# Kernel optimization log

Measured on AMD Instinct MI355X. Metric: run time of the kernel, lower is better.

## Reference

```python
import jax, jax.numpy as jnp
import numpy as np

B, D, M, C = 8192, 2048, 8, 1000

def setup_inputs() -> dict:
    key = jax.random.key(0)
    k1, k2, k3, k4, k5 = jax.random.split(key, 5)
    scale = 1.0 / np.sqrt(D)
    return {
        "x": jax.random.normal(k1, (B, D), dtype=jnp.float32),
        "model_weights": jax.random.normal(k2, (M, D, C), dtype=jnp.float32) * scale,
        "model_bias": jax.random.normal(k3, (M, C), dtype=jnp.float32) * 0.01,
        "resnet_weight": jax.random.normal(k4, (D, M * C), dtype=jnp.float32) * scale,
        "resnet_bias": jax.random.normal(k5, (M * C,), dtype=jnp.float32) * 0.01,
    }

def reference(x, model_weights, model_bias, resnet_weight, resnet_bias):
    # Per-submodel logits: [B, M, C]
    outputs = jnp.einsum("bd,mdc->bmc", x, model_weights) + model_bias[None, :, :]
    # Fusion weights from the weighting network: [B, M, C]
    w = (x @ resnet_weight + resnet_bias).reshape(x.shape[0], model_weights.shape[0], model_weights.shape[2])
    # Fused weighted sum over models (replaces the triple Python loop): [B, C]
    result = jnp.sum(outputs * w, axis=1)
    return result
```

## Files before the change

kernel.cpp:

```cpp
#include <hip/hip_runtime.h>
#include <hip/hip_bf16.h>
#include <stdint.h>

#define BDIM 8192
#define DDIM 2048
#define MDIM 8
#define CDIM 1000
#define CPAD 1024
#define NPAD 8192

typedef __attribute__((ext_vector_type(8))) short bf16x8;
typedef __attribute__((ext_vector_type(4))) float f32x4;

__device__ __forceinline__ unsigned short f2bf(float f) {
    union { float f; unsigned u; } v; v.f = f;
    unsigned r = v.u + 0x7fffu + ((v.u >> 16) & 1u);
    return (unsigned short)(r >> 16);
}

__device__ __forceinline__ void gl_lds16(const void* g, void* l) {
    __builtin_amdgcn_global_load_lds(
        (const __attribute__((address_space(1))) void*)g,
        (__attribute__((address_space(3))) void*)l,
        16, 0, 0);
}

__global__ void cast_x_kernel(const float4* __restrict__ x, ushort* __restrict__ xb) {
    int i = blockIdx.x * blockDim.x + threadIdx.x;
    float4 v = x[i];
    ushort4 o;
    o.x = f2bf(v.x); o.y = f2bf(v.y); o.z = f2bf(v.z); o.w = f2bf(v.w);
    *(ushort4*)&xb[(size_t)i * 4] = o;
}

__global__ void prep_w(const float* __restrict__ MW, ushort* __restrict__ wb) {
    __shared__ float tile[32][33];
    int m  = blockIdx.z;
    int c0 = blockIdx.x * 32;
    int d0 = blockIdx.y * 32;
    int tx = threadIdx.x, ty = threadIdx.y;
    const float* src = MW + (size_t)m * DDIM * CDIM;
#pragma unroll
    for (int i = 0; i < 4; i++) {
        int d = d0 + ty + i * 8;
        int c = c0 + tx;
        tile[ty + i * 8][tx] = (c < CDIM) ? src[(size_t)d * CDIM + c] : 0.f;
    }
    __syncthreads();
#pragma unroll
    for (int i = 0; i < 4; i++) {
        int c = c0 + ty + i * 8;
        int d = d0 + tx;
        wb[(size_t)(c * 8 + m) * DDIM + d] = f2bf(tile[tx][ty + i * 8]);
    }
}

__global__ void prep_r(const float* __restrict__ R, ushort* __restrict__ rb) {
    __shared__ float tile[32][33];
    int m  = blockIdx.z;
    int c0 = blockIdx.x * 32;
    int d0 = blockIdx.y * 32;
    int tx = threadIdx.x, ty = threadIdx.y;
#pragma unroll
    for (int i = 0; i < 4; i++) {
        int d = d0 + ty + i * 8;
        int c = c0 + tx;
        tile[ty + i * 8][tx] = (c < CDIM) ? R[(size_t)d * (MDIM * CDIM) + m * CDIM + c] : 0.f;
    }
    __syncthreads();
#pragma unroll
    for (int i = 0; i < 4; i++) {
        int c = c0 + ty + i * 8;
        int d = d0 + tx;
        rb[(size_t)(c * 8 + m) * DDIM + d] = f2bf(tile[tx][ty + i * 8]);
    }
}

__global__ void prep_bias(const float* __restrict__ mb, const float* __restrict__ rbv,
                          float* __restrict__ mb2, float* __restrict__ rb2) {
    int n = blockIdx.x * 256 + threadIdx.x;
    int c = n >> 3, m = n & 7;
    mb2[n] = (c < CDIM) ? mb[m * CDIM + c] : 0.f;
    rb2[n] = (c < CDIM) ? rbv[m * CDIM + c] : 0.f;
}

#define BM 256
#define BN 128
#define BK 64
#define NT (DDIM / BK)

#define STAGE(G, L) do {                                                       \
    _Pragma("unroll")                                                          \
    for (int it_ = 0; it_ < 2; ++it_) {                                        \
        int ci_ = it_ * 512 + tid;                                             \
        int r_ = ci_ >> 3, cc_ = ci_ & 7;                                      \
        gl_lds16((G) + (size_t)r_ * DDIM + (size_t)((cc_ ^ (r_ & 7)) << 3),    \
                 (L) + (size_t)(it_ * 512 + wbase) * 8);                       \
    }                                                                          \
} while (0)

#define LDA_K(AC, H, KH) do {                                                  \
    _Pragma("unroll")                                                          \
    for (int i_ = 0; i_ < 4; i_++) {                                           \
        int row_ = (H) * 128 + wm * 64 + i_ * 16 + (lane & 15);                \
        int cc_ = (KH) * 4 + (lane >> 4);                                      \
        af[i_][KH] = *(const bf16x8*)&(AC)[row_ * BK + ((cc_ ^ (row_ & 7)) << 3)]; \
    }                                                                          \
} while (0)

#define LDB_K(BS, BF, KH) do {                                                 \
    _Pragma("unroll")                                                          \
    for (int j_ = 0; j_ < 2; j_++) {                                           \
        int row_ = wn * 32 + j_ * 16 + (lane & 15);                            \
        int cc_ = (KH) * 4 + (lane >> 4);                                      \
        BF[j_][KH] = *(const bf16x8*)&(BS)[row_ * BK + ((cc_ ^ (row_ & 7)) << 3)]; \
    }                                                                          \
} while (0)

#define MMK(ACC, H, BF, KH) do {                                               \
    _Pragma("unroll")                                                          \
    for (int i_ = 0; i_ < 4; i_++)                                             \
    _Pragma("unroll")                                                          \
    for (int j_ = 0; j_ < 2; j_++)                                             \
        ACC[(H) * 4 + i_][j_] = __builtin_amdgcn_mfma_f32_16x16x32_bf16(       \
            af[i_][KH], BF[j_][KH], ACC[(H) * 4 + i_][j_], 0, 0, 0);           \
} while (0)

#define FENCE() asm volatile("" ::: "memory")
#define BARRIER() do { FENCE(); __builtin_amdgcn_s_barrier(); FENCE(); } while (0)
#define WAITV(N) asm volatile("s_waitcnt vmcnt(" #N ")" ::: "memory")
#define SP1() __builtin_amdgcn_s_setprio(1)
#define SP0() __builtin_amdgcn_s_setprio(0)

__global__ __launch_bounds__(512, 2) void gemm_fused(
    const ushort* __restrict__ xb, const ushort* __restrict__ wb,
    const ushort* __restrict__ rb,
    const float* __restrict__ mb2, const float* __restrict__ rb2,
    float* __restrict__ out) {
    __shared__ ushort As[2][BM * BK];
    __shared__ ushort B1s[2][BN * BK];
    __shared__ ushort B2s[2][BN * BK];

    int tid   = threadIdx.x;
    int lane  = tid & 63;
    int wid   = tid >> 6;
    int wm    = wid >> 2;
    int wn    = wid & 3;
    int wbase = tid & ~63;

    int wg = blockIdx.x;
    int wgs = (wg & 7) * 256 + (wg >> 3);
    int tile_m = wgs >> 6;
    int tile_n = wgs & 63;
    int brow = tile_m * BM;
    int bn0  = tile_n * BN;

    const ushort* xg  = xb + (size_t)brow * DDIM;
    const ushort* w1g = wb + (size_t)bn0 * DDIM;
    const ushort* w2g = rb + (size_t)bn0 * DDIM;

    f32x4 acc1[8][2] = {};
    f32x4 acc2[8][2] = {};
    bf16x8 af[4][2], bf1[2][2], bf2[2][2];

    STAGE(xg,               As[0]);
    STAGE(w1g,              B1s[0]);
    STAGE(w2g,              B2s[0]);
    STAGE(xg + 128 * DDIM,  As[0] + 128 * BK);
    STAGE(xg + BK,          As[1]);
    WAITV(4);
    BARRIER();

#pragma unroll 2
    for (int t = 0; t < NT; ++t) {
        int buf = t & 1;
        ushort* Ac  = As[buf];
        ushort* B1c = B1s[buf];
        ushort* B2c = B2s[buf];
        ushort* An  = As[buf ^ 1];
        ushort* B1n = B1s[buf ^ 1];
        ushort* B2n = B2s[buf ^ 1];
        const int kn  = (t + 1) * BK;
        const int kn2 = (t + 2) * BK;

        LDA_K(Ac, 0, 0);
        LDB_K(B1c, bf1, 0);
        LDB_K(B2c, bf2, 0);
        STAGE(w1g + kn, B1n);
        BARRIER();
        SP1(); MMK(acc1, 0, bf1, 0); MMK(acc2, 0, bf2, 0); SP0();
        BARRIER();

        LDA_K(Ac, 0, 1);
        LDB_K(B1c, bf1, 1);
        LDB_K(B2c, bf2, 1);
        STAGE(w2g + kn, B2n);
        SP1();
        WAITV(4);
        BARRIER();
        MMK(acc1, 0, bf1, 1); MMK(acc2, 0, bf2, 1); SP0();
        BARRIER();

        LDA_K(Ac, 1, 0);
        LDA_K(Ac, 1, 1);
        STAGE(xg + 128 * DDIM + kn, An + 128 * BK);
        BARRIER();
        SP1(); MMK(acc1, 1, bf1, 0); MMK(acc1, 1, bf1, 1); SP0();
        BARRIER();

        STAGE(xg + kn2, Ac);
        BARRIER();
        SP1(); MMK(acc2, 1, bf2, 0); MMK(acc2, 1, bf2, 1);
        WAITV(4);
        SP0();
        BARRIER();
    }
    WAITV(0);

#pragma unroll
    for (int j = 0; j < 2; j++) {
        int np = bn0 + wn * 32 + j * 16 + (lane & 15);
        float bb1 = mb2[np];
        float bb2 = rb2[np];
        int c = tile_n * 16 + wn * 4 + j * 2 + ((lane >> 3) & 1);
#pragma unroll
        for (int rf = 0; rf < 8; rf++) {
#pragma unroll
            for (int r = 0; r < 4; r++) {
                float p = (acc1[rf][j][r] + bb1) * (acc2[rf][j][r] + bb2);
                p += __shfl_xor(p, 1);
                p += __shfl_xor(p, 2);
                p += __shfl_xor(p, 4);
                if ((lane & 7) == 0 && c < CDIM) {
                    int row = brow + (rf >> 2) * 128 + wm * 64 + (rf & 3) * 16
                              + ((lane >> 4) << 2) + r;
                    out[(size_t)row * CDIM + c] = p;
                }
            }
        }
    }
}

extern "C" void kernel_launch(void* const* d_in, const int* in_sizes, int n_in,
                              void* d_out, int out_size, void* d_ws, size_t ws_size,
                              hipStream_t stream) {
    const float* x   = (const float*)d_in[0];
    const float* mw  = (const float*)d_in[1];
    const float* mb  = (const float*)d_in[2];
    const float* rw  = (const float*)d_in[3];
    const float* rbv = (const float*)d_in[4];
    float* out = (float*)d_out;

    char* ws = (char*)d_ws;
    ushort* xb  = (ushort*)ws;
    ushort* wb  = (ushort*)(ws + (size_t)33554432);
    ushort* rb  = (ushort*)(ws + (size_t)67108864);
    float*  mb2 = (float*)(ws + (size_t)100663296);
    float*  rb2 = (float*)(ws + (size_t)100696064);

    cast_x_kernel<<<BDIM * DDIM / (256 * 4), 256, 0, stream>>>((const float4*)x, xb);
    prep_w<<<dim3(CPAD / 32, DDIM / 32, MDIM), dim3(32, 8), 0, stream>>>(mw, wb);
    prep_r<<<dim3(CPAD / 32, DDIM / 32, MDIM), dim3(32, 8), 0, stream>>>(rw, rb);
    prep_bias<<<NPAD / 256, 256, 0, stream>>>(mb, rbv, mb2, rb2);

    gemm_fused<<<dim3((BDIM / BM) * (NPAD / BN)), 512, 0, stream>>>(xb, wb, rb, mb2, rb2, out);
}
```

Measured before the change: 592.8 us.

## Switch fused GEMM to 32x32x16 MFMA tiles and restage pipeline

Replaces the 16x16x32 bf16 MFMA fragments with 32x32x16 MFMAs, which cuts the number of LDS fragment loads per unit of math and uses larger accumulator vectors. The per-iteration schedule is reorganised into four phases, each issuing one global-to-LDS stage and one MFMA block. The A tile is no longer prefetched two steps ahead; it is staged one step ahead into the alternate buffer. The epilogue is remapped to the 32x32 accumulator layout. This relies on the wait counts and barriers still being correct for the new order, and it may change register pressure under the two-blocks-per-CU launch bound.

```diff
diff --git a/kernel.cpp b/kernel.cpp
--- a/kernel.cpp
+++ b/kernel.cpp
@@ -11,6 +11,7 @@
 
 typedef __attribute__((ext_vector_type(8))) short bf16x8;
 typedef __attribute__((ext_vector_type(4))) float f32x4;
+typedef __attribute__((ext_vector_type(16))) float f32x16;
 
 __device__ __forceinline__ unsigned short f2bf(float f) {
     union { float f; unsigned u; } v; v.f = f;
@@ -99,38 +100,41 @@
     }                                                                          \
 } while (0)
 
-#define LDA_K(AC, H, KH) do {                                                  \
-    _Pragma("unroll")                                                          \
-    for (int i_ = 0; i_ < 4; i_++) {                                           \
-        int row_ = (H) * 128 + wm * 64 + i_ * 16 + (lane & 15);                \
-        int cc_ = (KH) * 4 + (lane >> 4);                                      \
-        af[i_][KH] = *(const bf16x8*)&(AC)[row_ * BK + ((cc_ ^ (row_ & 7)) << 3)]; \
-    }                                                                          \
-} while (0)
-
-#define LDB_K(BS, BF, KH) do {                                                 \
-    _Pragma("unroll")                                                          \
-    for (int j_ = 0; j_ < 2; j_++) {                                           \
-        int row_ = wn * 32 + j_ * 16 + (lane & 15);                            \
-        int cc_ = (KH) * 4 + (lane >> 4);                                      \
-        BF[j_][KH] = *(const bf16x8*)&(BS)[row_ * BK + ((cc_ ^ (row_ & 7)) << 3)]; \
-    }                                                                          \
-} while (0)
-
-#define MMK(ACC, H, BF, KH) do {                                               \
-    _Pragma("unroll")                                                          \
-    for (int i_ = 0; i_ < 4; i_++)                                             \
-    _Pragma("unroll")                                                          \
-    for (int j_ = 0; j_ < 2; j_++)                                             \
-        ACC[(H) * 4 + i_][j_] = __builtin_amdgcn_mfma_f32_16x16x32_bf16(       \
-            af[i_][KH], BF[j_][KH], ACC[(H) * 4 + i_][j_], 0, 0, 0);           \
+#define LDA32(AC, H, KH0) do {                                                 \
+    _Pragma("unroll")                                                          \
+    for (int i2_ = 0; i2_ < 2; i2_++)                                          \
+    _Pragma("unroll")                                                          \
+    for (int q_ = 0; q_ < 2; q_++) {                                           \
+        int row_ = (H) * 128 + wm * 64 + i2_ * 32 + (lane & 31);               \
+        int cc_ = ((KH0) + q_) * 2 + (lane >> 5);                              \
+        af[i2_][q_] = *(const bf16x8*)&(AC)[row_ * BK + ((cc_ ^ (row_ & 7)) << 3)]; \
+    }                                                                          \
+} while (0)
+
+#define LDB32(BS, BF, KH0) do {                                                \
+    _Pragma("unroll")                                                          \
+    for (int q_ = 0; q_ < 2; q_++) {                                           \
+        int row_ = wn * 32 + (lane & 31);                                      \
+        int cc_ = ((KH0) + q_) * 2 + (lane >> 5);                              \
+        BF[q_] = *(const bf16x8*)&(BS)[row_ * BK + ((cc_ ^ (row_ & 7)) << 3)]; \
+    }                                                                          \
+} while (0)
+
+#define MM32(H) do {                                                           \
+    __builtin_amdgcn_s_setprio(1);                                             \
+    _Pragma("unroll")                                                          \
+    for (int q_ = 0; q_ < 2; q_++) {                                           \
+        acc1[(H)*2+0] = __builtin_amdgcn_mfma_f32_32x32x16_bf16(af[0][q_], bf1[q_], acc1[(H)*2+0], 0, 0, 0); \
+        acc1[(H)*2+1] = __builtin_amdgcn_mfma_f32_32x32x16_bf16(af[1][q_], bf1[q_], acc1[(H)*2+1], 0, 0, 0); \
+        acc2[(H)*2+0] = __builtin_amdgcn_mfma_f32_32x32x16_bf16(af[0][q_], bf2[q_], acc2[(H)*2+0], 0, 0, 0); \
+        acc2[(H)*2+1] = __builtin_amdgcn_mfma_f32_32x32x16_bf16(af[1][q_], bf2[q_], acc2[(H)*2+1], 0, 0, 0); \
+    }                                                                          \
+    __builtin_amdgcn_s_setprio(0);                                             \
 } while (0)
 
 #define FENCE() asm volatile("" ::: "memory")
 #define BARRIER() do { FENCE(); __builtin_amdgcn_s_barrier(); FENCE(); } while (0)
 #define WAITV(N) asm volatile("s_waitcnt vmcnt(" #N ")" ::: "memory")
-#define SP1() __builtin_amdgcn_s_setprio(1)
-#define SP0() __builtin_amdgcn_s_setprio(0)
 
 __global__ __launch_bounds__(512, 2) void gemm_fused(
     const ushort* __restrict__ xb, const ushort* __restrict__ wb,
@@ -159,16 +163,15 @@
     const ushort* w1g = wb + (size_t)bn0 * DDIM;
     const ushort* w2g = rb + (size_t)bn0 * DDIM;
 
-    f32x4 acc1[8][2] = {};
-    f32x4 acc2[8][2] = {};
-    bf16x8 af[4][2], bf1[2][2], bf2[2][2];
+    f32x16 acc1[4] = {};
+    f32x16 acc2[4] = {};
+    bf16x8 af[2][2], bf1[2], bf2[2];
 
     STAGE(xg,               As[0]);
     STAGE(w1g,              B1s[0]);
     STAGE(w2g,              B2s[0]);
     STAGE(xg + 128 * DDIM,  As[0] + 128 * BK);
-    STAGE(xg + BK,          As[1]);
-    WAITV(4);
+    WAITV(2);
     BARRIER();
 
 #pragma unroll 2
@@ -180,60 +183,60 @@
         ushort* An  = As[buf ^ 1];
         ushort* B1n = B1s[buf ^ 1];
         ushort* B2n = B2s[buf ^ 1];
-        const int kn  = (t + 1) * BK;
-        const int kn2 = (t + 2) * BK;
-
-        LDA_K(Ac, 0, 0);
-        LDB_K(B1c, bf1, 0);
-        LDB_K(B2c, bf2, 0);
+        const int kn = (t + 1) * BK;
+
+        LDA32(Ac, 0, 0);
+        LDB32(B1c, bf1, 0);
+        LDB32(B2c, bf2, 0);
+        STAGE(xg + kn, An);
+        BARRIER();
+        MM32(0);
+        BARRIER();
+
+        LDA32(Ac, 0, 2);
+        LDB32(B1c, bf1, 2);
+        LDB32(B2c, bf2, 2);
         STAGE(w1g + kn, B1n);
         BARRIER();
-        SP1(); MMK(acc1, 0, bf1, 0); MMK(acc2, 0, bf2, 0); SP0();
-        BARRIER();
-
-        LDA_K(Ac, 0, 1);
-        LDB_K(B1c, bf1, 1);
-        LDB_K(B2c, bf2, 1);
+        MM32(0);
+        WAITV(4);
+        BARRIER();
+
+        LDA32(Ac, 1, 0);
+        LDB32(B1c, bf1, 0);
+        LDB32(B2c, bf2, 0);
         STAGE(w2g + kn, B2n);
-        SP1();
-        WAITV(4);
-        BARRIER();
-        MMK(acc1, 0, bf1, 1); MMK(acc2, 0, bf2, 1); SP0();
-        BARRIER();
-
-        LDA_K(Ac, 1, 0);
-        LDA_K(Ac, 1, 1);
+        BARRIER();
+        MM32(1);
+        BARRIER();
+
+        LDA32(Ac, 1, 2);
+        LDB32(B1c, bf1, 2);
+        LDB32(B2c, bf2, 2);
         STAGE(xg + 128 * DDIM + kn, An + 128 * BK);
         BARRIER();
-        SP1(); MMK(acc1, 1, bf1, 0); MMK(acc1, 1, bf1, 1); SP0();
-        BARRIER();
-
-        STAGE(xg + kn2, Ac);
-        BARRIER();
-        SP1(); MMK(acc2, 1, bf2, 0); MMK(acc2, 1, bf2, 1);
-        WAITV(4);
-        SP0();
+        MM32(1);
+        WAITV(2);
         BARRIER();
     }
     WAITV(0);
 
-#pragma unroll
-    for (int j = 0; j < 2; j++) {
-        int np = bn0 + wn * 32 + j * 16 + (lane & 15);
+    {
+        int np = bn0 + wn * 32 + (lane & 31);
         float bb1 = mb2[np];
         float bb2 = rb2[np];
-        int c = tile_n * 16 + wn * 4 + j * 2 + ((lane >> 3) & 1);
-#pragma unroll
-        for (int rf = 0; rf < 8; rf++) {
-#pragma unroll
-            for (int r = 0; r < 4; r++) {
-                float p = (acc1[rf][j][r] + bb1) * (acc2[rf][j][r] + bb2);
+        int c = tile_n * 16 + wn * 4 + ((lane & 31) >> 3);
+#pragma unroll
+        for (int fi = 0; fi < 4; fi++) {
+#pragma unroll
+            for (int r = 0; r < 16; r++) {
+                float p = (acc1[fi][r] + bb1) * (acc2[fi][r] + bb2);
                 p += __shfl_xor(p, 1);
                 p += __shfl_xor(p, 2);
                 p += __shfl_xor(p, 4);
                 if ((lane & 7) == 0 && c < CDIM) {
-                    int row = brow + (rf >> 2) * 128 + wm * 64 + (rf & 3) * 16
-                              + ((lane >> 4) << 2) + r;
+                    int row = brow + (fi >> 1) * 128 + wm * 64 + (fi & 1) * 32
+                              + (r & 3) + 8 * (r >> 2) + 4 * (lane >> 5);
                     out[(size_t)row * CDIM + c] = p;
                 }
             }
```

Measured after the change: 685.2 us. +15.6%, slower.
